# Optimization experiments

Measured on AMD Instinct MI355X. Metric: run time of the kernel, lower is better.

The kernel has to match this reference:

```python
import jax, jax.numpy as jnp
import numpy as np

N_NODES = 50000
N_EDGES = 600000
IN_DIM = 128
HID = 128
OUT_DIM = 10
N_GRAPHS = 512
LN_EPS = 1e-5
N_CELLS = 4  # len(macro_architecture) + 1


def setup_inputs() -> dict:
    key = jax.random.key(0)
    ks = jax.random.split(key, 8)
    s = 0.05
    x = jax.random.normal(ks[0], (N_NODES, IN_DIM), dtype=jnp.float32)
    edge_index = jax.random.randint(ks[1], (2, N_EDGES), 0, N_NODES, dtype=jnp.int32)
    batch = jnp.sort(jax.random.randint(ks[2], (N_NODES,), 0, N_GRAPHS, dtype=jnp.int32))
    return {
        "x": x,
        "edge_index": edge_index,
        "batch": batch,
        "W_pre": jax.random.normal(ks[3], (IN_DIM, HID), dtype=jnp.float32) * s,
        "b_pre": jnp.zeros((HID,), jnp.float32),
        "conv_W": jax.random.normal(ks[4], (N_CELLS, HID, HID), dtype=jnp.float32) * s,
        "conv_b": jnp.zeros((N_CELLS, HID), jnp.float32),
        "ln_g": jnp.ones((N_CELLS, HID), jnp.float32),
        "ln_b": jnp.zeros((N_CELLS, HID), jnp.float32),
        "W_post": jax.random.normal(ks[5], (HID, OUT_DIM), dtype=jnp.float32) * s,
        "b_post": jnp.zeros((OUT_DIM,), jnp.float32),
    }


def _gcn_conv(x, W, b, src, dst):
    """GCNConv: add self-loops, symmetric deg^-1/2 normalization, gather-scatter."""
    n = x.shape[0]
    h = x @ W                                   # [N, HID]
    loops = jnp.arange(n, dtype=src.dtype)
    s = jnp.concatenate([src, loops])           # [E + N]
    d = jnp.concatenate([dst, loops])
    deg = jax.ops.segment_sum(jnp.ones_like(d, jnp.float32), d, num_segments=n)
    dinv = jax.lax.rsqrt(jnp.maximum(deg, 1.0))  # deg >= 1 via self-loops
    coef = dinv[s] * dinv[d]                    # [E + N]
    out = jax.ops.segment_sum(h[s] * coef[:, None], d, num_segments=n)
    return out + b


def _layer_norm(x, g, b):
    mu = jnp.mean(x, axis=-1, keepdims=True)
    var = jnp.var(x, axis=-1, keepdims=True)
    return (x - mu) * jax.lax.rsqrt(var + LN_EPS) * g + b


def _cell(x, i, conv_W, conv_b, ln_g, ln_b, src, dst):
    h = _gcn_conv(x, conv_W[i], conv_b[i], src, dst)
    return jax.nn.relu(_layer_norm(h, ln_g[i], ln_b[i]))


def reference(x, edge_index, batch, W_pre, b_pre, conv_W, conv_b, ln_g, ln_b, W_post, b_post):
    src, dst = edge_index[0], edge_index[1]
    # pre MLP
    h0 = x @ W_pre + b_pre
    # state node 0 (all 3 outgoing edges active -> identical output reused)
    n0 = _cell(h0, 0, conv_W, conv_b, ln_g, ln_b, src, dst)
    # state node 1: input = node0's output
    n1 = _cell(n0, 1, conv_W, conv_b, ln_g, ln_b, src, dst)
    # second-to-last node: sum of [-2] outputs (n0, n1)
    s2l = _cell(n0 + n1, 2, conv_W, conv_b, ln_g, ln_b, src, dst)
    # last node: sum of [-1] outputs (n0, n1) + second-to-last output
    last = _cell(n0 + n1 + s2l, 3, conv_W, conv_b, ln_g, ln_b, src, dst)
    # sum pooling by graph id, then post MLP
    pooled = jax.ops.segment_sum(last, batch, num_segments=N_GRAPHS)  # [G, HID]
    return pooled @ W_post + b_post
```

## Files before the change

kernel.cpp:

```cpp
#include <hip/hip_runtime.h>

#define HID 128
#define LN_EPS 1e-5f

using f32x4 = __attribute__((ext_vector_type(4))) float;
using s16x8 = __attribute__((ext_vector_type(8))) short;

__device__ inline float bl2f(unsigned u) { u <<= 16; return __builtin_bit_cast(float, u); }
__device__ inline float bh2f(unsigned u) { u &= 0xffff0000u; return __builtin_bit_cast(float, u); }
__device__ inline float sb2f(short s) {
  unsigned u = ((unsigned)(unsigned short)s) << 16;
  return __builtin_bit_cast(float, u);
}
__device__ inline unsigned f2b_bits(float f) {
  unsigned u = __builtin_bit_cast(unsigned, f);
  return (u + 0x7fffu + ((u >> 16) & 1u)) >> 16;
}
__device__ inline short f2b(float f) { return (short)f2b_bits(f); }
__device__ inline unsigned pack2(float a, float b) { return f2b_bits(a) | (f2b_bits(b) << 16); }

__device__ inline void addu4(const uint4 u, float a[8]) {
  a[0] += bl2f(u.x); a[1] += bh2f(u.x);
  a[2] += bl2f(u.y); a[3] += bh2f(u.y);
  a[4] += bl2f(u.z); a[5] += bh2f(u.z);
  a[6] += bl2f(u.w); a[7] += bh2f(u.w);
}


__global__ __launch_bounds__(64) void prep_w_kernel(const float* __restrict__ W_pre,
                                                    const float* __restrict__ conv_W,
                                                    short* __restrict__ Wt) {
  int b = blockIdx.x;
  int w = b >> 7, n = b & 127;
  const float* W = (w == 0) ? W_pre : conv_W + (size_t)(w - 1) * HID * HID;
  int t = threadIdx.x;
  float f0 = W[(2 * t) * HID + n];
  float f1 = W[(2 * t + 1) * HID + n];
  ((unsigned*)Wt)[(size_t)(w * HID + n) * 64 + t] = pack2(f0, f1);
}


__global__ void zero_ints_kernel(int* __restrict__ p, int n) {
  int i = blockIdx.x * blockDim.x + threadIdx.x;
  if (i < n) p[i] = 0;
}

__global__ void deg_count_kernel(const int* __restrict__ dst, int E, int* __restrict__ deg) {
  int e = blockIdx.x * blockDim.x + threadIdx.x;
  if (e < E) atomicAdd(&deg[dst[e]], 1);
}

__global__ __launch_bounds__(256) void alloc_kernel(const int* __restrict__ deg,
                                                    int* __restrict__ start,
                                                    int* __restrict__ cur,
                                                    float* __restrict__ dinv,
                                                    int* __restrict__ cnt, int n) {
  __shared__ int wt[4];
  __shared__ int bbase;
  int t = threadIdx.x, lane = t & 63, wid = t >> 6;
  int i = blockIdx.x * 256 + t;
  int d = (i < n) ? deg[i] : 0;
  int x = d;
  #pragma unroll
  for (int off = 1; off < 64; off <<= 1) {
    int u = __shfl_up(x, off, 64);
    if (lane >= off) x += u;
  }
  if (lane == 63) wt[wid] = x;
  __syncthreads();
  if (t == 0) bbase = atomicAdd(cnt, wt[0] + wt[1] + wt[2] + wt[3]);
  __syncthreads();
  int wbase = bbase;
  for (int w = 0; w < wid; ++w) wbase += wt[w];
  int excl = wbase + x - d;
  if (i < n) {
    start[i] = excl;
    cur[i] = excl;
    dinv[i] = rsqrtf((float)(d + 1));
  }
}

__global__ void fill_csr_kernel(const int* __restrict__ src, const int* __restrict__ dst,
                                int E, int* __restrict__ cur, int* __restrict__ col) {
  int e = blockIdx.x * blockDim.x + threadIdx.x;
  if (e < E) {
    int d = dst[e];
    int p = atomicAdd(&cur[d], 1);
    col[p] = src[e];
  }
}


template<bool AF32>
__global__ __launch_bounds__(256) void gemm_mfma_kernel(
    const void* __restrict__ Xv, const short* __restrict__ Wt,
    const float* __restrict__ bias, const float* __restrict__ dinv,
    short* __restrict__ Y, int M) {
  __shared__ short lds[4 * 32 * HID];
  int t = threadIdx.x;
  int wave = t >> 6, l = t & 63;
  int lg = l >> 4, lr = l & 15;
  int mb = blockIdx.x * 128 + wave * 32;

  const f32x4 z4 = {0.f, 0.f, 0.f, 0.f};
  f32x4 acc[2][8];
  #pragma unroll
  for (int i = 0; i < 2; ++i)
    #pragma unroll
    for (int j = 0; j < 8; ++j) acc[i][j] = z4;

  const short* Xb = (const short*)Xv;
  const float* Xf = (const float*)Xv;

  #pragma unroll
  for (int kk = 0; kk < 4; ++kk) {
    int k0 = kk * 32 + lg * 8;
    s16x8 a[2];
    #pragma unroll
    for (int mf = 0; mf < 2; ++mf) {
      int row = mb + mf * 16 + lr;
      s16x8 av = {0, 0, 0, 0, 0, 0, 0, 0};
      if (row < M) {
        if constexpr (AF32) {
          const float4* p = (const float4*)(Xf + (size_t)row * HID + k0);
          float4 x0 = p[0], x1 = p[1];
          av[0] = f2b(x0.x); av[1] = f2b(x0.y); av[2] = f2b(x0.z); av[3] = f2b(x0.w);
          av[4] = f2b(x1.x); av[5] = f2b(x1.y); av[6] = f2b(x1.z); av[7] = f2b(x1.w);
        } else {
          av = *(const s16x8*)(Xb + (size_t)row * HID + k0);
        }
      }
      a[mf] = av;
    }
    #pragma unroll
    for (int nf = 0; nf < 8; ++nf) {
      s16x8 b = *(const s16x8*)(Wt + (size_t)(nf * 16 + lr) * HID + k0);
      acc[0][nf] = __builtin_amdgcn_mfma_f32_16x16x32_bf16(a[0], b, acc[0][nf], 0, 0, 0);
      acc[1][nf] = __builtin_amdgcn_mfma_f32_16x16x32_bf16(a[1], b, acc[1][nf], 0, 0, 0);
    }
  }

  float bv[8];
  #pragma unroll
  for (int nf = 0; nf < 8; ++nf) bv[nf] = bias ? bias[nf * 16 + lr] : 0.f;

  short* wsl = lds + wave * 32 * HID;
  #pragma unroll
  for (int mf = 0; mf < 2; ++mf) {
    #pragma unroll
    for (int r = 0; r < 4; ++r) {
      int ri = mf * 16 + lg * 4 + r;
      int row = mb + ri;
      float dv = 1.f;
      if (dinv && row < M) dv = dinv[row];
      #pragma unroll
      for (int nf = 0; nf < 8; ++nf) {
        float v = (acc[mf][nf][r] + bv[nf]) * dv;
        wsl[ri * HID + nf * 16 + lr] = f2b(v);
      }
    }
  }
  __syncthreads();

  #pragma unroll
  for (int it = 0; it < 8; ++it) {
    int ro = it * 4 + lg;
    int row = mb + ro;
    s16x8 v = *(const s16x8*)(wsl + it * 512 + l * 8);
    if (row < M) *(s16x8*)(Y + (size_t)row * HID + lr * 8) = v;
  }
}


__global__ __launch_bounds__(512) void cell_kernel(
    const short* __restrict__ Sin, const int* __restrict__ start,
    const int* __restrict__ deg, const float* __restrict__ dinv,
    const int* __restrict__ col, const short* __restrict__ Wt,
    const float* __restrict__ bconv, const float* __restrict__ lng,
    const float* __restrict__ lnb, short* __restrict__ Sout,
    int N, int mode) {
  __shared__ short Zs[16 * HID];
  __shared__ float red[16][8][2];
  int t = threadIdx.x;
  int wave = t >> 6, l = t & 63, lr = l & 15, sub = l >> 4;
  int lg = sub;
  const uint4* GR = (const uint4*)Sin;

  #pragma unroll
  for (int s2 = 0; s2 < 2; ++s2) {
    int rowL = wave * 2 + s2;
    int v = blockIdx.x * 16 + rowL;
    int zofs = rowL * HID + ((lr * 8) ^ ((rowL & 7) << 3));
    if (v >= N) {
      if (sub == 0) *(uint4*)&Zs[zofs] = make_uint4(0u, 0u, 0u, 0u);
      continue;
    }
    float a[8] = {0.f, 0.f, 0.f, 0.f, 0.f, 0.f, 0.f, 0.f};
    if (sub == 0) addu4(GR[(size_t)v * 16 + lr], a);
    int lo = start[v], hi = lo + deg[v];
    int j = lo;
    for (; j + 8 <= hi; j += 8) {
      int c0 = col[j + sub];
      int c1 = col[j + 4 + sub];
      uint4 u0 = GR[(size_t)c0 * 16 + lr];
      uint4 u1 = GR[(size_t)c1 * 16 + lr];
      addu4(u0, a);
      addu4(u1, a);
    }
    for (; j < hi; j += 4)
      if (j + sub < hi) addu4(GR[(size_t)col[j + sub] * 16 + lr], a);

    #pragma unroll
    for (int i = 0; i < 8; ++i) {
      a[i] += __shfl_xor(a[i], 16, 64);
      a[i] += __shfl_xor(a[i], 32, 64);
    }
    float d = dinv[v];
    if (sub == 0) {
      uint4 q;
      q.x = pack2(a[0] * d, a[1] * d); q.y = pack2(a[2] * d, a[3] * d);
      q.z = pack2(a[4] * d, a[5] * d); q.w = pack2(a[6] * d, a[7] * d);
      *(uint4*)&Zs[zofs] = q;
    }
  }
  __syncthreads();

  f32x4 acc = {0.f, 0.f, 0.f, 0.f};
  #pragma unroll
  for (int kk = 0; kk < 4; ++kk) {
    int k0 = kk * 32 + lg * 8;
    s16x8 af = *(const s16x8*)&Zs[lr * HID + (k0 ^ ((lr & 7) << 3))];
    s16x8 bf = *(const s16x8*)(Wt + (size_t)(wave * 16 + lr) * HID + k0);
    acc = __builtin_amdgcn_mfma_f32_16x16x32_bf16(af, bf, acc, 0, 0, 0);
  }
  int c = wave * 16 + lr;
  float bc = bconv[c];
  float h[4], s1[4], s2v[4];
  #pragma unroll
  for (int r = 0; r < 4; ++r) {
    h[r] = acc[r] + bc;
    s1[r] = h[r];
    s2v[r] = h[r] * h[r];
  }
  #pragma unroll
  for (int off = 1; off <= 8; off <<= 1) {
    #pragma unroll
    for (int r = 0; r < 4; ++r) {
      s1[r] += __shfl_xor(s1[r], off, 64);
      s2v[r] += __shfl_xor(s2v[r], off, 64);
    }
  }
  if (lr == 0) {
    #pragma unroll
    for (int r = 0; r < 4; ++r) {
      red[lg * 4 + r][wave][0] = s1[r];
      red[lg * 4 + r][wave][1] = s2v[r];
    }
  }
  __syncthreads();
  float gl = lng[c], bl = lnb[c];
  #pragma unroll
  for (int r = 0; r < 4; ++r) {
    int row = lg * 4 + r;
    const float4* rp = (const float4*)&red[row][0][0];
    float t1 = 0.f, t2 = 0.f;
    #pragma unroll
    for (int q4 = 0; q4 < 4; ++q4) {
      float4 vv = rp[q4];
      t1 += vv.x + vv.z;
      t2 += vv.y + vv.w;
    }
    float mu = t1 * (1.f / HID);
    float var = t2 * (1.f / HID) - mu * mu;
    float inv = rsqrtf(fmaxf(var, 0.f) + LN_EPS);
    float yv = fmaxf(fmaf((h[r] - mu) * inv, gl, bl), 0.f);
    Zs[row * HID + (c ^ ((row & 7) << 3))] = f2b(yv);
  }
  __syncthreads();

  if (t < 256) {
    int row = t >> 4, q = t & 15;
    int v = blockIdx.x * 16 + row;
    if (v < N) {
      s16x8 y8 = *(const s16x8*)&Zs[row * HID + ((q * 8) ^ ((row & 7) << 3))];
      float yv[8];
      #pragma unroll
      for (int i = 0; i < 8; ++i) yv[i] = sb2f(y8[i]);
      uint4 o;
      if (mode == 2) {
        o.x = pack2(yv[0], yv[1]); o.y = pack2(yv[2], yv[3]);
        o.z = pack2(yv[4], yv[5]); o.w = pack2(yv[6], yv[7]);
      } else if (mode == 0) {
        float d = dinv[v];
        o.x = pack2(yv[0] * d, yv[1] * d); o.y = pack2(yv[2] * d, yv[3] * d);
        o.z = pack2(yv[4] * d, yv[5] * d); o.w = pack2(yv[6] * d, yv[7] * d);
      } else {
        float d = dinv[v];
        uint4 ui = GR[(size_t)v * 16 + q];
        o.x = pack2(bl2f(ui.x) + yv[0] * d, bh2f(ui.x) + yv[1] * d);
        o.y = pack2(bl2f(ui.y) + yv[2] * d, bh2f(ui.y) + yv[3] * d);
        o.z = pack2(bl2f(ui.z) + yv[4] * d, bh2f(ui.z) + yv[5] * d);
        o.w = pack2(bl2f(ui.w) + yv[6] * d, bh2f(ui.w) + yv[7] * d);
      }
      ((uint4*)Sout)[(size_t)v * 16 + q] = o;
    }
  }
}


__device__ inline int lower_bound_i(const int* a, int n, int key) {
  int lo = 0, hi = n;
  while (lo < hi) { int m = (lo + hi) >> 1; if (a[m] < key) lo = m + 1; else hi = m; }
  return lo;
}

__global__ __launch_bounds__(128) void pool_post_kernel(
    const short* __restrict__ Yl, const int* __restrict__ batch, int n,
    const float* __restrict__ Wp, const float* __restrict__ bp,
    float* __restrict__ out, int n_out) {
  int g = blockIdx.x, t = threadIdx.x;
  int wave = t >> 6;
  int lr = t & 15, slot = t >> 4;
  int lo = lower_bound_i(batch, n, g);
  int hi = lower_bound_i(batch, n, g + 1);
  const uint4* YR = (const uint4*)Yl;
  float a[8] = {0.f, 0.f, 0.f, 0.f, 0.f, 0.f, 0.f, 0.f};
  for (int r = lo + slot; r < hi; r += 8) addu4(YR[(size_t)r * 16 + lr], a);
  #pragma unroll
  for (int i = 0; i < 8; ++i) {
    a[i] += __shfl_xor(a[i], 16, 64);
    a[i] += __shfl_xor(a[i], 32, 64);
  }
  __shared__ float ls[2][HID];
  if ((slot & 3) == 0) {
    #pragma unroll
    for (int i = 0; i < 8; ++i) ls[wave][8 * lr + i] = a[i];
  }
  __syncthreads();
  if (t < n_out) {
    float o = bp[t];
    #pragma unroll 8
    for (int k = 0; k < HID; ++k) o = fmaf(ls[0][k] + ls[1][k], Wp[k * n_out + t], o);
    out[g * n_out + t] = o;
  }
}


extern "C" void kernel_launch(void* const* d_in, const int* in_sizes, int n_in,
                              void* d_out, int out_size, void* d_ws, size_t ws_size,
                              hipStream_t stream) {
  const float* x      = (const float*)d_in[0];
  const int*   ei     = (const int*)d_in[1];
  const int*   batch  = (const int*)d_in[2];
  const float* W_pre  = (const float*)d_in[3];
  const float* b_pre  = (const float*)d_in[4];
  const float* conv_W = (const float*)d_in[5];
  const float* conv_b = (const float*)d_in[6];
  const float* ln_g   = (const float*)d_in[7];
  const float* ln_b   = (const float*)d_in[8];
  const float* W_post = (const float*)d_in[9];
  const float* b_post = (const float*)d_in[10];
  float* out = (float*)d_out;

  const int N = in_sizes[2];
  const int E = in_sizes[1] / 2;
  const int OUT_DIM = 10;
  const int NG = out_size / OUT_DIM;

  char* p = (char*)d_ws;
  short* SA  = (short*)p;            p += (size_t)N * HID * 2;
  short* SB  = (short*)p;            p += (size_t)N * HID * 2;
  short* Wt  = (short*)p;            p += (size_t)5 * HID * HID * 2;
  float* dinv = (float*)p;           p += (size_t)N * 4;
  int* deg   = (int*)p;              p += (size_t)(N + 1) * 4;
  int* startv = (int*)p;             p += (size_t)N * 4;
  int* cur   = (int*)p;              p += (size_t)N * 4;
  int* col   = (int*)p;              p += (size_t)E * 4;
  int* cnt   = deg + N;

  const int* srcp = ei;
  const int* dstp = ei + E;

  int nb256 = (N + 255) / 256;
  int eb256 = (E + 255) / 256;
  int gemm_grid = (N + 127) / 128;
  int cell_grid = (N + 15) / 16;

  prep_w_kernel<<<5 * HID, 64, 0, stream>>>(W_pre, conv_W, Wt);

  zero_ints_kernel<<<nb256, 256, 0, stream>>>(deg, N + 1);
  deg_count_kernel<<<eb256, 256, 0, stream>>>(dstp, E, deg);
  alloc_kernel<<<nb256, 256, 0, stream>>>(deg, startv, cur, dinv, cnt, N);
  fill_csr_kernel<<<eb256, 256, 0, stream>>>(srcp, dstp, E, cur, col);

  gemm_mfma_kernel<true><<<gemm_grid, 256, 0, stream>>>(x, Wt + 0 * 16384, b_pre, dinv, SA, N);

  cell_kernel<<<cell_grid, 512, 0, stream>>>(SA, startv, deg, dinv, col, Wt + 1 * 16384,
                                             conv_b + 0 * HID, ln_g + 0 * HID, ln_b + 0 * HID,
                                             SB, N, 0);
  cell_kernel<<<cell_grid, 512, 0, stream>>>(SB, startv, deg, dinv, col, Wt + 2 * 16384,
                                             conv_b + 1 * HID, ln_g + 1 * HID, ln_b + 1 * HID,
                                             SA, N, 1);
  cell_kernel<<<cell_grid, 512, 0, stream>>>(SA, startv, deg, dinv, col, Wt + 3 * 16384,
                                             conv_b + 2 * HID, ln_g + 2 * HID, ln_b + 2 * HID,
                                             SB, N, 1);
  cell_kernel<<<cell_grid, 512, 0, stream>>>(SB, startv, deg, dinv, col, Wt + 4 * 16384,
                                             conv_b + 3 * HID, ln_g + 3 * HID, ln_b + 3 * HID,
                                             SA, N, 2);

  pool_post_kernel<<<NG, 128, 0, stream>>>(SA, batch, N, W_post, b_post, out, OUT_DIM);
}
```

Before: 298.3 us.

## Degree-sort nodes and assign one 16-lane group per node in cell kernel

Adds a counting sort of nodes by in-degree (histogram, prefix, scatter into a permutation) so each cell block processes nodes of similar degree. The gather now maps one 16-lane group to each node, walking its edges sequentially with packed float2 accumulation, instead of four groups splitting one node's edges and reducing with cross-lane shuffles. Blocks now cover 32 rows, with two MFMA tiles per wave. This removes shuffle reductions and load imbalance within a wave, but adds three small preprocessing kernels and indirect perm lookups, and scatters output writes in degree order rather than node order.

```diff
diff --git a/kernel.cpp b/kernel.cpp
--- a/kernel.cpp
+++ b/kernel.cpp
@@ -3,6 +3,7 @@
 #define HID 128
 #define LN_EPS 1e-5f
 
+using f32x2 = __attribute__((ext_vector_type(2))) float;
 using f32x4 = __attribute__((ext_vector_type(4))) float;
 using s16x8 = __attribute__((ext_vector_type(8))) short;
 
@@ -18,12 +19,8 @@
 }
 __device__ inline short f2b(float f) { return (short)f2b_bits(f); }
 __device__ inline unsigned pack2(float a, float b) { return f2b_bits(a) | (f2b_bits(b) << 16); }
-
-__device__ inline void addu4(const uint4 u, float a[8]) {
-  a[0] += bl2f(u.x); a[1] += bh2f(u.x);
-  a[2] += bl2f(u.y); a[3] += bh2f(u.y);
-  a[4] += bl2f(u.z); a[5] += bh2f(u.z);
-  a[6] += bl2f(u.w); a[7] += bh2f(u.w);
+__device__ inline f32x2 up2(unsigned u) {
+  f32x2 r; r.x = bl2f(u); r.y = bh2f(u); return r;
 }
 
 
@@ -90,10 +87,38 @@
   }
 }
 
-
-template<bool AF32>
+__global__ void hist_kernel(const int* __restrict__ deg, int* __restrict__ hist, int n) {
+  int i = blockIdx.x * blockDim.x + threadIdx.x;
+  if (i < n) atomicAdd(&hist[min(deg[i], 63)], 1);
+}
+
+__global__ __launch_bounds__(64) void binoff_kernel(const int* __restrict__ hist,
+                                                    int* __restrict__ bincur) {
+  int lane = threadIdx.x;
+  int rb = 63 - lane;
+  int v = hist[rb];
+  int x = v;
+  #pragma unroll
+  for (int off = 1; off < 64; off <<= 1) {
+    int u = __shfl_up(x, off, 64);
+    if (lane >= off) x += u;
+  }
+  bincur[rb] = x - v;
+}
+
+__global__ void scatter_kernel(const int* __restrict__ deg, int* __restrict__ bincur,
+                               int* __restrict__ perm, int n) {
+  int i = blockIdx.x * blockDim.x + threadIdx.x;
+  if (i < n) {
+    int b = min(deg[i], 63);
+    int p = atomicAdd(&bincur[b], 1);
+    perm[p] = i;
+  }
+}
+
+
 __global__ __launch_bounds__(256) void gemm_mfma_kernel(
-    const void* __restrict__ Xv, const short* __restrict__ Wt,
+    const float* __restrict__ Xf, const short* __restrict__ Wt,
     const float* __restrict__ bias, const float* __restrict__ dinv,
     short* __restrict__ Y, int M) {
   __shared__ short lds[4 * 32 * HID];
@@ -109,9 +134,6 @@
     #pragma unroll
     for (int j = 0; j < 8; ++j) acc[i][j] = z4;
 
-  const short* Xb = (const short*)Xv;
-  const float* Xf = (const float*)Xv;
-
   #pragma unroll
   for (int kk = 0; kk < 4; ++kk) {
     int k0 = kk * 32 + lg * 8;
@@ -121,14 +143,10 @@
       int row = mb + mf * 16 + lr;
       s16x8 av = {0, 0, 0, 0, 0, 0, 0, 0};
       if (row < M) {
-        if constexpr (AF32) {
-          const float4* p = (const float4*)(Xf + (size_t)row * HID + k0);
-          float4 x0 = p[0], x1 = p[1];
-          av[0] = f2b(x0.x); av[1] = f2b(x0.y); av[2] = f2b(x0.z); av[3] = f2b(x0.w);
-          av[4] = f2b(x1.x); av[5] = f2b(x1.y); av[6] = f2b(x1.z); av[7] = f2b(x1.w);
-        } else {
-          av = *(const s16x8*)(Xb + (size_t)row * HID + k0);
-        }
+        const float4* p = (const float4*)(Xf + (size_t)row * HID + k0);
+        float4 x0 = p[0], x1 = p[1];
+        av[0] = f2b(x0.x); av[1] = f2b(x0.y); av[2] = f2b(x0.z); av[3] = f2b(x0.w);
+        av[4] = f2b(x1.x); av[5] = f2b(x1.y); av[6] = f2b(x1.z); av[7] = f2b(x1.w);
       }
       a[mf] = av;
     }
@@ -142,7 +160,7 @@
 
   float bv[8];
   #pragma unroll
-  for (int nf = 0; nf < 8; ++nf) bv[nf] = bias ? bias[nf * 16 + lr] : 0.f;
+  for (int nf = 0; nf < 8; ++nf) bv[nf] = bias[nf * 16 + lr];
 
   short* wsl = lds + wave * 32 * HID;
   #pragma unroll
@@ -151,8 +169,7 @@
     for (int r = 0; r < 4; ++r) {
       int ri = mf * 16 + lg * 4 + r;
       int row = mb + ri;
-      float dv = 1.f;
-      if (dinv && row < M) dv = dinv[row];
+      float dv = (row < M) ? dinv[row] : 1.f;
       #pragma unroll
       for (int nf = 0; nf < 8; ++nf) {
         float v = (acc[mf][nf][r] + bv[nf]) * dv;
@@ -175,114 +192,122 @@
 __global__ __launch_bounds__(512) void cell_kernel(
     const short* __restrict__ Sin, const int* __restrict__ start,
     const int* __restrict__ deg, const float* __restrict__ dinv,
-    const int* __restrict__ col, const short* __restrict__ Wt,
-    const float* __restrict__ bconv, const float* __restrict__ lng,
-    const float* __restrict__ lnb, short* __restrict__ Sout,
-    int N, int mode) {
-  __shared__ short Zs[16 * HID];
-  __shared__ float red[16][8][2];
+    const int* __restrict__ col, const int* __restrict__ perm,
+    const short* __restrict__ Wt, const float* __restrict__ bconv,
+    const float* __restrict__ lng, const float* __restrict__ lnb,
+    short* __restrict__ Sout, int N, int mode) {
+  __shared__ short Zs[32 * HID];
+  __shared__ float red[32][8][2];
   int t = threadIdx.x;
   int wave = t >> 6, l = t & 63, lr = l & 15, sub = l >> 4;
-  int lg = sub;
   const uint4* GR = (const uint4*)Sin;
 
-  #pragma unroll
-  for (int s2 = 0; s2 < 2; ++s2) {
-    int rowL = wave * 2 + s2;
-    int v = blockIdx.x * 16 + rowL;
-    int zofs = rowL * HID + ((lr * 8) ^ ((rowL & 7) << 3));
-    if (v >= N) {
-      if (sub == 0) *(uint4*)&Zs[zofs] = make_uint4(0u, 0u, 0u, 0u);
-      continue;
-    }
-    float a[8] = {0.f, 0.f, 0.f, 0.f, 0.f, 0.f, 0.f, 0.f};
-    if (sub == 0) addu4(GR[(size_t)v * 16 + lr], a);
+  int rowL = wave * 4 + sub;
+  int slot = blockIdx.x * 32 + rowL;
+  int v = (slot < N) ? perm[slot] : -1;
+  int zofs = rowL * HID + ((lr * 8) ^ ((rowL & 7) << 3));
+  if (v >= 0) {
+    uint4 us = GR[(size_t)v * 16 + lr];
+    f32x2 a0 = up2(us.x), a1 = up2(us.y), a2 = up2(us.z), a3 = up2(us.w);
     int lo = start[v], hi = lo + deg[v];
     int j = lo;
-    for (; j + 8 <= hi; j += 8) {
-      int c0 = col[j + sub];
-      int c1 = col[j + 4 + sub];
+    for (; j + 1 < hi; j += 2) {
+      int c0 = col[j], c1 = col[j + 1];
       uint4 u0 = GR[(size_t)c0 * 16 + lr];
       uint4 u1 = GR[(size_t)c1 * 16 + lr];
-      addu4(u0, a);
-      addu4(u1, a);
-    }
-    for (; j < hi; j += 4)
-      if (j + sub < hi) addu4(GR[(size_t)col[j + sub] * 16 + lr], a);
-
-    #pragma unroll
-    for (int i = 0; i < 8; ++i) {
-      a[i] += __shfl_xor(a[i], 16, 64);
-      a[i] += __shfl_xor(a[i], 32, 64);
+      a0 += up2(u0.x); a1 += up2(u0.y); a2 += up2(u0.z); a3 += up2(u0.w);
+      a0 += up2(u1.x); a1 += up2(u1.y); a2 += up2(u1.z); a3 += up2(u1.w);
+    }
+    if (j < hi) {
+      uint4 u0 = GR[(size_t)col[j] * 16 + lr];
+      a0 += up2(u0.x); a1 += up2(u0.y); a2 += up2(u0.z); a3 += up2(u0.w);
     }
     float d = dinv[v];
-    if (sub == 0) {
-      uint4 q;
-      q.x = pack2(a[0] * d, a[1] * d); q.y = pack2(a[2] * d, a[3] * d);
-      q.z = pack2(a[4] * d, a[5] * d); q.w = pack2(a[6] * d, a[7] * d);
-      *(uint4*)&Zs[zofs] = q;
-    }
-  }
-  __syncthreads();
-
-  f32x4 acc = {0.f, 0.f, 0.f, 0.f};
+    uint4 q;
+    q.x = pack2(a0.x * d, a0.y * d);
+    q.y = pack2(a1.x * d, a1.y * d);
+    q.z = pack2(a2.x * d, a2.y * d);
+    q.w = pack2(a3.x * d, a3.y * d);
+    *(uint4*)&Zs[zofs] = q;
+  } else {
+    *(uint4*)&Zs[zofs] = make_uint4(0u, 0u, 0u, 0u);
+  }
+  __syncthreads();
+
+  f32x4 accA = {0.f, 0.f, 0.f, 0.f}, accB = {0.f, 0.f, 0.f, 0.f};
   #pragma unroll
   for (int kk = 0; kk < 4; ++kk) {
-    int k0 = kk * 32 + lg * 8;
-    s16x8 af = *(const s16x8*)&Zs[lr * HID + (k0 ^ ((lr & 7) << 3))];
+    int k0 = kk * 32 + sub * 8;
     s16x8 bf = *(const s16x8*)(Wt + (size_t)(wave * 16 + lr) * HID + k0);
-    acc = __builtin_amdgcn_mfma_f32_16x16x32_bf16(af, bf, acc, 0, 0, 0);
+    s16x8 afA = *(const s16x8*)&Zs[lr * HID + (k0 ^ ((lr & 7) << 3))];
+    s16x8 afB = *(const s16x8*)&Zs[(16 + lr) * HID + (k0 ^ ((lr & 7) << 3))];
+    accA = __builtin_amdgcn_mfma_f32_16x16x32_bf16(afA, bf, accA, 0, 0, 0);
+    accB = __builtin_amdgcn_mfma_f32_16x16x32_bf16(afB, bf, accB, 0, 0, 0);
   }
   int c = wave * 16 + lr;
   float bc = bconv[c];
-  float h[4], s1[4], s2v[4];
+  float hA[4], hB[4], s1A[4], s2A[4], s1B[4], s2B[4];
   #pragma unroll
   for (int r = 0; r < 4; ++r) {
-    h[r] = acc[r] + bc;
-    s1[r] = h[r];
-    s2v[r] = h[r] * h[r];
+    hA[r] = accA[r] + bc; s1A[r] = hA[r]; s2A[r] = hA[r] * hA[r];
+    hB[r] = accB[r] + bc; s1B[r] = hB[r]; s2B[r] = hB[r] * hB[r];
   }
   #pragma unroll
   for (int off = 1; off <= 8; off <<= 1) {
     #pragma unroll
     for (int r = 0; r < 4; ++r) {
-      s1[r] += __shfl_xor(s1[r], off, 64);
-      s2v[r] += __shfl_xor(s2v[r], off, 64);
+      s1A[r] += __shfl_xor(s1A[r], off, 64);
+      s2A[r] += __shfl_xor(s2A[r], off, 64);
+      s1B[r] += __shfl_xor(s1B[r], off, 64);
+      s2B[r] += __shfl_xor(s2B[r], off, 64);
     }
   }
   if (lr == 0) {
     #pragma unroll
     for (int r = 0; r < 4; ++r) {
-      red[lg * 4 + r][wave][0] = s1[r];
-      red[lg * 4 + r][wave][1] = s2v[r];
+      red[sub * 4 + r][wave][0] = s1A[r];
+      red[sub * 4 + r][wave][1] = s2A[r];
+      red[16 + sub * 4 + r][wave][0] = s1B[r];
+      red[16 + sub * 4 + r][wave][1] = s2B[r];
     }
   }
   __syncthreads();
   float gl = lng[c], bl = lnb[c];
   #pragma unroll
   for (int r = 0; r < 4; ++r) {
-    int row = lg * 4 + r;
-    const float4* rp = (const float4*)&red[row][0][0];
-    float t1 = 0.f, t2 = 0.f;
-    #pragma unroll
-    for (int q4 = 0; q4 < 4; ++q4) {
-      float4 vv = rp[q4];
-      t1 += vv.x + vv.z;
-      t2 += vv.y + vv.w;
-    }
-    float mu = t1 * (1.f / HID);
-    float var = t2 * (1.f / HID) - mu * mu;
-    float inv = rsqrtf(fmaxf(var, 0.f) + LN_EPS);
-    float yv = fmaxf(fmaf((h[r] - mu) * inv, gl, bl), 0.f);
-    Zs[row * HID + (c ^ ((row & 7) << 3))] = f2b(yv);
-  }
-  __syncthreads();
-
-  if (t < 256) {
-    int row = t >> 4, q = t & 15;
-    int v = blockIdx.x * 16 + row;
-    if (v < N) {
-      s16x8 y8 = *(const s16x8*)&Zs[row * HID + ((q * 8) ^ ((row & 7) << 3))];
+    {
+      int row = sub * 4 + r;
+      const float4* rp = (const float4*)&red[row][0][0];
+      float t1 = 0.f, t2 = 0.f;
+      #pragma unroll
+      for (int q4 = 0; q4 < 4; ++q4) { float4 vv = rp[q4]; t1 += vv.x + vv.z; t2 += vv.y + vv.w; }
+      float mu = t1 * (1.f / HID);
+      float var = t2 * (1.f / HID) - mu * mu;
+      float inv = rsqrtf(fmaxf(var, 0.f) + LN_EPS);
+      float yv = fmaxf(fmaf((hA[r] - mu) * inv, gl, bl), 0.f);
+      Zs[row * HID + (c ^ ((row & 7) << 3))] = f2b(yv);
+    }
+    {
+      int row = 16 + sub * 4 + r;
+      const float4* rp = (const float4*)&red[row][0][0];
+      float t1 = 0.f, t2 = 0.f;
+      #pragma unroll
+      for (int q4 = 0; q4 < 4; ++q4) { float4 vv = rp[q4]; t1 += vv.x + vv.z; t2 += vv.y + vv.w; }
+      float mu = t1 * (1.f / HID);
+      float var = t2 * (1.f / HID) - mu * mu;
+      float inv = rsqrtf(fmaxf(var, 0.f) + LN_EPS);
+      float yv = fmaxf(fmaf((hB[r] - mu) * inv, gl, bl), 0.f);
+      Zs[row * HID + (c ^ ((row & 7) << 3))] = f2b(yv);
+    }
+  }
+  __syncthreads();
+
+  {
+    int row = t >> 4, qq = t & 15;
+    int slot2 = blockIdx.x * 32 + row;
+    if (slot2 < N) {
+      int v2 = perm[slot2];
+      s16x8 y8 = *(const s16x8*)&Zs[row * HID + ((qq * 8) ^ ((row & 7) << 3))];
       float yv[8];
       #pragma unroll
       for (int i = 0; i < 8; ++i) yv[i] = sb2f(y8[i]);
@@ -291,18 +316,18 @@
         o.x = pack2(yv[0], yv[1]); o.y = pack2(yv[2], yv[3]);
         o.z = pack2(yv[4], yv[5]); o.w = pack2(yv[6], yv[7]);
       } else if (mode == 0) {
-        float d = dinv[v];
+        float d = dinv[v2];
         o.x = pack2(yv[0] * d, yv[1] * d); o.y = pack2(yv[2] * d, yv[3] * d);
         o.z = pack2(yv[4] * d, yv[5] * d); o.w = pack2(yv[6] * d, yv[7] * d);
       } else {
-        float d = dinv[v];
-        uint4 ui = GR[(size_t)v * 16 + q];
+        float d = dinv[v2];
+        uint4 ui = GR[(size_t)v2 * 16 + qq];
         o.x = pack2(bl2f(ui.x) + yv[0] * d, bh2f(ui.x) + yv[1] * d);
         o.y = pack2(bl2f(ui.y) + yv[2] * d, bh2f(ui.y) + yv[3] * d);
         o.z = pack2(bl2f(ui.z) + yv[4] * d, bh2f(ui.z) + yv[5] * d);
         o.w = pack2(bl2f(ui.w) + yv[6] * d, bh2f(ui.w) + yv[7] * d);
       }
-      ((uint4*)Sout)[(size_t)v * 16 + q] = o;
+      ((uint4*)Sout)[(size_t)v2 * 16 + qq] = o;
     }
   }
 }
@@ -325,7 +350,13 @@
   int hi = lower_bound_i(batch, n, g + 1);
   const uint4* YR = (const uint4*)Yl;
   float a[8] = {0.f, 0.f, 0.f, 0.f, 0.f, 0.f, 0.f, 0.f};
-  for (int r = lo + slot; r < hi; r += 8) addu4(YR[(size_t)r * 16 + lr], a);
+  for (int r = lo + slot; r < hi; r += 8) {
+    uint4 u = YR[(size_t)r * 16 + lr];
+    a[0] += bl2f(u.x); a[1] += bh2f(u.x);
+    a[2] += bl2f(u.y); a[3] += bh2f(u.y);
+    a[4] += bl2f(u.z); a[5] += bh2f(u.z);
+    a[6] += bl2f(u.w); a[7] += bh2f(u.w);
+  }
   #pragma unroll
   for (int i = 0; i < 8; ++i) {
     a[i] += __shfl_xor(a[i], 16, 64);
@@ -376,6 +407,9 @@
   int* startv = (int*)p;             p += (size_t)N * 4;
   int* cur   = (int*)p;              p += (size_t)N * 4;
   int* col   = (int*)p;              p += (size_t)E * 4;
+  int* perm  = (int*)p;              p += (size_t)N * 4;
+  int* hist  = (int*)p;              p += 64 * 4;
+  int* bincur = (int*)p;             p += 64 * 4;
   int* cnt   = deg + N;
 
   const int* srcp = ei;
@@ -384,27 +418,31 @@
   int nb256 = (N + 255) / 256;
   int eb256 = (E + 255) / 256;
   int gemm_grid = (N + 127) / 128;
-  int cell_grid = (N + 15) / 16;
+  int cell_grid = (N + 31) / 32;
 
   prep_w_kernel<<<5 * HID, 64, 0, stream>>>(W_pre, conv_W, Wt);
 
   zero_ints_kernel<<<nb256, 256, 0, stream>>>(deg, N + 1);
+  zero_ints_kernel<<<1, 64, 0, stream>>>(hist, 64);
   deg_count_kernel<<<eb256, 256, 0, stream>>>(dstp, E, deg);
   alloc_kernel<<<nb256, 256, 0, stream>>>(deg, startv, cur, dinv, cnt, N);
   fill_csr_kernel<<<eb256, 256, 0, stream>>>(srcp, dstp, E, cur, col);
-
-  gemm_mfma_kernel<true><<<gemm_grid, 256, 0, stream>>>(x, Wt + 0 * 16384, b_pre, dinv, SA, N);
-
-  cell_kernel<<<cell_grid, 512, 0, stream>>>(SA, startv, deg, dinv, col, Wt + 1 * 16384,
+  hist_kernel<<<nb256, 256, 0, stream>>>(deg, hist, N);
+  binoff_kernel<<<1, 64, 0, stream>>>(hist, bincur);
+  scatter_kernel<<<nb256, 256, 0, stream>>>(deg, bincur, perm, N);
+
+  gemm_mfma_kernel<<<gemm_grid, 256, 0, stream>>>(x, Wt + 0 * 16384, b_pre, dinv, SA, N);
+
+  cell_kernel<<<cell_grid, 512, 0, stream>>>(SA, startv, deg, dinv, col, perm, Wt + 1 * 16384,
                                              conv_b + 0 * HID, ln_g + 0 * HID, ln_b + 0 * HID,
                                              SB, N, 0);
-  cell_kernel<<<cell_grid, 512, 0, stream>>>(SB, startv, deg, dinv, col, Wt + 2 * 16384,
+  cell_kernel<<<cell_grid, 512, 0, stream>>>(SB, startv, deg, dinv, col, perm, Wt + 2 * 16384,
                                              conv_b + 1 * HID, ln_g + 1 * HID, ln_b + 1 * HID,
                                              SA, N, 1);
-  cell_kernel<<<cell_grid, 512, 0, stream>>>(SA, startv, deg, dinv, col, Wt + 3 * 16384,
+  cell_kernel<<<cell_grid, 512, 0, stream>>>(SA, startv, deg, dinv, col, perm, Wt + 3 * 16384,
                                              conv_b + 2 * HID, ln_g + 2 * HID, ln_b + 2 * HID,
                                              SB, N, 1);
-  cell_kernel<<<cell_grid, 512, 0, stream>>>(SB, startv, deg, dinv, col, Wt + 4 * 16384,
+  cell_kernel<<<cell_grid, 512, 0, stream>>>(SB, startv, deg, dinv, col, perm, Wt + 4 * 16384,
                                              conv_b + 3 * HID, ln_g + 3 * HID, ln_b + 3 * HID,
                                              SA, N, 2);
 
```

Result: slower. 568.7 us (+90.7%).
